# Optimization experiments

Hardware: AMD Instinct MI355X
Metric: run time of the kernel (lower is better)

The kernel has to match this reference:

```python
import jax, jax.numpy as jnp
import numpy as np

B, S, F = 64, 4096, 128      # batch, seq_len, fcnn_unit
RANK, FUSED = 16, 10


def setup_inputs() -> dict:
    key = jax.random.key(0)
    ks = jax.random.split(key, 10)
    xavier = lambda k, shape: jax.random.normal(k, shape, jnp.float32) * np.sqrt(2.0 / (shape[-2] + shape[-1]))
    return {
        "imu_h": jax.random.normal(ks[0], (B, S, F), jnp.float32),
        "vid_h": jax.random.normal(ks[1], (B, S, F), jnp.float32),
        "anthro": jax.random.uniform(ks[2], (B, 1, 2), jnp.float32, 0.5, 1.5),
        "imu_factor": xavier(ks[3], (RANK, 1, F + 1, FUSED)),
        "vid_factor": xavier(ks[4], (RANK, 1, F + 1, FUSED)),
        "fusion_weights": xavier(ks[5], (1, RANK)),
        "fusion_bias": jnp.zeros((1, FUSED), jnp.float32),
        "W1": xavier(ks[6], (FUSED, F)),
        "b1": jnp.zeros((F,), jnp.float32),
        "W2": xavier(ks[7], (F, 2)),
        "b2": jnp.zeros((2,), jnp.float32),
    }


def reference(imu_h, vid_h, anthro, imu_factor, vid_factor,
              fusion_weights, fusion_bias, W1, b1, W2, b2):
    b, s, _ = imu_h.shape
    ones = jnp.ones((b, s, 1), imu_h.dtype)
    _imu_h = jnp.concatenate([ones, imu_h], axis=2)   # [B,S,F+1]
    _vid_h = jnp.concatenate([ones, vid_h], axis=2)
    # torch.matmul([B,S,F+1], [rank,1,F+1,d]) -> [rank,B,S,d]
    fusion_imu = jnp.einsum('bsf,rfd->rbsd', _imu_h, imu_factor[:, 0])
    fusion_vid = jnp.einsum('bsf,rfd->rbsd', _vid_h, vid_factor[:, 0])
    fusion_zy = fusion_imu * fusion_vid               # [rank,B,S,d]
    # weighted combine over rank + bias -> [B,S,d]
    seq = jnp.einsum('r,rbsd->bsd', fusion_weights[0], fusion_zy) + fusion_bias[0]
    seq = jax.nn.relu(seq @ W1 + b1)                  # [B,S,F]
    seq = seq @ W2 + b2                               # [B,S,2]
    wh = (anthro[:, 0, 0] * anthro[:, 0, 1])[:, None, None]  # weight*height
    return seq / wh
```

## Files before the change

### kernel.cpp

```cpp
#include <hip/hip_runtime.h>
#include <hip/hip_bf16.h>
#include <stdint.h>


#define NTOK   262144
#define FDIM   128
#define RANKN  16
#define FUSED  10
#define WTE    (FUSED*RANKN*FDIM)
#define NEXTRA 1984

typedef unsigned short u16;
typedef __bf16 bf16x8 __attribute__((ext_vector_type(8)));
typedef float  f32x4  __attribute__((ext_vector_type(4)));

static __device__ __forceinline__ u16 f2bf(float f) {
    union { float f; uint32_t u; } c; c.f = f;
    uint32_t u = c.u + 0x7FFFu + ((c.u >> 16) & 1u);
    return (u16)(u >> 16);
}

__global__ void prep_kernel(const float* __restrict__ imf, const float* __restrict__ vif,
                            const float* __restrict__ fw,  const float* __restrict__ fb,
                            const float* __restrict__ W1,  const float* __restrict__ b1,
                            const float* __restrict__ W2,
                            u16* __restrict__ wImu, u16* __restrict__ wVid,
                            float* __restrict__ extra) {
    int idx = blockIdx.x * blockDim.x + threadIdx.x;
    float* a0  = extra;
    float* b0  = extra + 160;
    float* W1L = extra + 320;
    float* b1L = extra + 1600;
    float* w20 = extra + 1728;
    float* w21 = extra + 1856;

    if (idx < FUSED * RANKN * FDIM) {
        int k = idx & 127;
        int r = (idx >> 7) & 15;
        int d = idx >> 11;
        int src = r * ((FDIM + 1) * FUSED) + (k + 1) * FUSED + d;
        int kk   = k >> 5;
        int quad = (k >> 3) & 3;
        int j    = k & 7;
        int lane = quad * 16 + r;
        int dst  = ((d * 4 + kk) * 64 + lane) * 8 + j;
        wImu[dst] = f2bf(fw[r] * imf[src]);
        wVid[dst] = f2bf(vif[src]);
    }
    if (idx < RANKN * FUSED) {
        int r = idx & 15, d = idx >> 4;
        int src = r * ((FDIM + 1) * FUSED) + d;
        a0[idx] = fw[r] * imf[src];
        b0[idx] = vif[src];
    }
    if (idx < 1280) {
        int i = idx & 3;
        int t = idx >> 2;
        int d = t % 10;
        int gq = t / 10;
        int g = gq >> 2, q = gq & 3;
        int j = q * 32 + g * 4 + i;
        W1L[idx] = W1[d * FDIM + j];
    }
    if (idx < FDIM) {
        int i = idx & 3;
        int gq = idx >> 2;
        int g = gq >> 2, q = gq & 3;
        int j = q * 32 + g * 4 + i;
        float acc = b1[j];
        #pragma unroll
        for (int d = 0; d < FUSED; ++d) acc += fb[d] * W1[d * FDIM + j];
        b1L[idx] = acc;
        w20[idx] = W2[2 * j];
        w21[idx] = W2[2 * j + 1];
    }
}

__launch_bounds__(512, 2)
__global__ void fusion_main(const float* __restrict__ imu, const float* __restrict__ vid,
                            const float* __restrict__ anthro,
                            const u16* __restrict__ wImuG, const u16* __restrict__ wVidG,
                            const float* __restrict__ extraG,
                            const float* __restrict__ b2g,
                            float* __restrict__ out) {
    extern __shared__ char smem[];
    u16* sFI = (u16*)smem;
    u16* sFV = sFI + WTE;
    float* sX   = (float*)(sFV + WTE);
    float* sA0  = sX;
    float* sB0  = sX + 160;
    float* sW1L = sX + 320;
    float* sB1L = sX + 1600;
    float* sW20 = sX + 1728;
    float* sW21 = sX + 1856;

    {
        const uint4* srcI = (const uint4*)wImuG;
        const uint4* srcV = (const uint4*)wVidG;
        const uint4* srcX = (const uint4*)extraG;
        uint4* dstI = (uint4*)sFI;
        uint4* dstV = (uint4*)sFV;
        uint4* dstX = (uint4*)sX;
        for (int i = threadIdx.x; i < WTE / 8; i += blockDim.x) {
            dstI[i] = srcI[i];
            dstV[i] = srcV[i];
        }
        for (int i = threadIdx.x; i < NEXTRA / 4; i += blockDim.x)
            dstX[i] = srcX[i];
    }

    const int lane = threadIdx.x & 63;
    const int quad = lane >> 4;
    const int r16  = lane & 15;
    const int wid  = threadIdx.x >> 6;
    const int t0   = (blockIdx.x * 8 + wid) * 16;

    const int bidx = t0 >> 12;
    const float invwh = 1.0f / (anthro[2 * bidx] * anthro[2 * bidx + 1]);
    const float b20 = b2g[0], b21 = b2g[1];

    bf16x8 aI[4], aV[4];
    {
        const float* baseI = imu + (size_t)(t0 + r16) * FDIM + quad * 8;
        const float* baseV = vid + (size_t)(t0 + r16) * FDIM + quad * 8;
        #pragma unroll
        for (int kk = 0; kk < 4; ++kk) {
            f32x4 v0 = *(const f32x4*)(baseI + kk * 32);
            f32x4 v1 = *(const f32x4*)(baseI + kk * 32 + 4);
            f32x4 w0 = *(const f32x4*)(baseV + kk * 32);
            f32x4 w1 = *(const f32x4*)(baseV + kk * 32 + 4);
            bf16x8 a, b;
            #pragma unroll
            for (int j = 0; j < 4; ++j) {
                a[j] = (__bf16)v0[j]; a[j + 4] = (__bf16)v1[j];
                b[j] = (__bf16)w0[j]; b[j + 4] = (__bf16)w1[j];
            }
            aI[kk] = a;
            aV[kk] = b;
        }
    }
    __syncthreads();

    const bf16x8* fragI = (const bf16x8*)(const void*)sFI;
    const bf16x8* fragV = (const bf16x8*)(const void*)sFV;

    float seqv[FUSED];
    #pragma unroll
    for (int d = 0; d < FUSED; ++d) {
        f32x4 accU = {0.f, 0.f, 0.f, 0.f};
        f32x4 accV = {0.f, 0.f, 0.f, 0.f};
        #pragma unroll
        for (int kk = 0; kk < 4; ++kk) {
            accU = __builtin_amdgcn_mfma_f32_16x16x32_bf16(fragI[(d * 4 + kk) * 64 + lane], aI[kk], accU, 0, 0, 0);
            accV = __builtin_amdgcn_mfma_f32_16x16x32_bf16(fragV[(d * 4 + kk) * 64 + lane], aV[kk], accV, 0, 0, 0);
        }
        f32x4 a0c = *(const f32x4*)(sA0 + d * 16 + quad * 4);
        f32x4 b0c = *(const f32x4*)(sB0 + d * 16 + quad * 4);
        float s = 0.f;
        #pragma unroll
        for (int reg = 0; reg < 4; ++reg)
            s += (accU[reg] + a0c[reg]) * (accV[reg] + b0c[reg]);
        s += __shfl_xor(s, 16, 64);
        s += __shfl_xor(s, 32, 64);
        seqv[d] = s;
    }

    float o0 = 0.f, o1 = 0.f;
    #pragma unroll
    for (int g = 0; g < 8; ++g) {
        const int gq = g * 4 + quad;
        f32x4 h = *(const f32x4*)(sB1L + gq * 4);
        #pragma unroll
        for (int d = 0; d < FUSED; ++d) {
            f32x4 wv = *(const f32x4*)(sW1L + (gq * 10 + d) * 4);
            #pragma unroll
            for (int i = 0; i < 4; ++i) h[i] += seqv[d] * wv[i];
        }
        f32x4 w20v = *(const f32x4*)(sW20 + gq * 4);
        f32x4 w21v = *(const f32x4*)(sW21 + gq * 4);
        #pragma unroll
        for (int i = 0; i < 4; ++i) {
            float hr = fmaxf(h[i], 0.f);
            o0 += hr * w20v[i];
            o1 += hr * w21v[i];
        }
    }
    o0 += __shfl_xor(o0, 16, 64);
    o0 += __shfl_xor(o0, 32, 64);
    o1 += __shfl_xor(o1, 16, 64);
    o1 += __shfl_xor(o1, 32, 64);

    if (lane < 16) {
        const int t = t0 + r16;
        float2 o = make_float2((o0 + b20) * invwh, (o1 + b21) * invwh);
        *(float2*)(out + 2 * t) = o;
    }
}

extern "C" void kernel_launch(void* const* d_in, const int* in_sizes, int n_in,
                              void* d_out, int out_size, void* d_ws, size_t ws_size,
                              hipStream_t stream) {
    const float* imu    = (const float*)d_in[0];
    const float* vid    = (const float*)d_in[1];
    const float* anthro = (const float*)d_in[2];
    const float* imf    = (const float*)d_in[3];
    const float* vif    = (const float*)d_in[4];
    const float* fw     = (const float*)d_in[5];
    const float* fb     = (const float*)d_in[6];
    const float* W1     = (const float*)d_in[7];
    const float* b1     = (const float*)d_in[8];
    const float* W2     = (const float*)d_in[9];
    const float* b2     = (const float*)d_in[10];
    float* out = (float*)d_out;

    u16* wImu = (u16*)d_ws;
    u16* wVid = wImu + WTE;
    float* extra = (float*)(wVid + WTE);

    prep_kernel<<<80, 256, 0, stream>>>(imf, vif, fw, fb, W1, b1, W2,
                                        wImu, wVid, extra);

    const size_t smem = (size_t)(2 * WTE) * sizeof(u16)
                      + (size_t)NEXTRA * sizeof(float);
    fusion_main<<<2048, 512, smem, stream>>>(imu, vid, anthro, wImu, wVid,
                                             extra, b2, out);
}
```

Before: 318.8 us.

## Switch to 32x32x16 MFMA with 32 tokens per wave

```diff
diff --git a/kernel.cpp b/kernel.cpp
--- a/kernel.cpp
+++ b/kernel.cpp
@@ -13,6 +13,7 @@
 typedef unsigned short u16;
 typedef __bf16 bf16x8 __attribute__((ext_vector_type(8)));
 typedef float  f32x4  __attribute__((ext_vector_type(4)));
+typedef float  f32x16 __attribute__((ext_vector_type(16)));
 
 static __device__ __forceinline__ u16 f2bf(float f) {
     union { float f; uint32_t u; } c; c.f = f;
@@ -35,38 +36,43 @@
     float* w21 = extra + 1856;
 
     if (idx < FUSED * RANKN * FDIM) {
-        int k = idx & 127;
-        int r = (idx >> 7) & 15;
-        int d = idx >> 11;
-        int src = r * ((FDIM + 1) * FUSED) + (k + 1) * FUSED + d;
-        int kk   = k >> 5;
-        int quad = (k >> 3) & 3;
-        int j    = k & 7;
-        int lane = quad * 16 + r;
-        int dst  = ((d * 4 + kk) * 64 + lane) * 8 + j;
-        wImu[dst] = f2bf(fw[r] * imf[src]);
-        wVid[dst] = f2bf(vif[src]);
-    }
-    if (idx < RANKN * FUSED) {
-        int r = idx & 15, d = idx >> 4;
-        int src = r * ((FDIM + 1) * FUSED) + d;
+        int j    = idx & 7;
+        int lane = (idx >> 3) & 63;
+        int ks   = (idx >> 9) & 7;
+        int nt   = idx >> 12;
+        int k    = ks * 16 + (lane >> 5) * 8 + j;
+        int col  = nt * 32 + (lane & 31);
+        int d    = nt * 2 + ((col >> 4) & 1);
+        int r    = col & 15;
+        int src  = r * ((FDIM + 1) * FUSED) + (k + 1) * FUSED + d;
+        wImu[idx] = f2bf(fw[r] * imf[src]);
+        wVid[idx] = f2bf(vif[src]);
+    }
+    if (idx < 160) {
+        int slot = idx & 7;
+        int hi   = (idx >> 3) & 1;
+        int dl   = (idx >> 4) & 1;
+        int nt   = idx >> 5;
+        int d    = nt * 2 + dl;
+        int r    = (slot & 3) + 8 * (slot >> 2) + 4 * hi;
+        int src  = r * ((FDIM + 1) * FUSED) + d;
         a0[idx] = fw[r] * imf[src];
         b0[idx] = vif[src];
     }
     if (idx < 1280) {
-        int i = idx & 3;
-        int t = idx >> 2;
-        int d = t % 10;
+        int i  = idx & 3;
+        int t  = idx >> 2;
+        int d  = t % 10;
         int gq = t / 10;
-        int g = gq >> 2, q = gq & 3;
-        int j = q * 32 + g * 4 + i;
+        int hi = gq >> 4, jg = gq & 15;
+        int j  = hi * 64 + jg * 4 + i;
         W1L[idx] = W1[d * FDIM + j];
     }
     if (idx < FDIM) {
-        int i = idx & 3;
+        int i  = idx & 3;
         int gq = idx >> 2;
-        int g = gq >> 2, q = gq & 3;
-        int j = q * 32 + g * 4 + i;
+        int hi = gq >> 4, jg = gq & 15;
+        int j  = hi * 64 + jg * 4 + i;
         float acc = b1[j];
         #pragma unroll
         for (int d = 0; d < FUSED; ++d) acc += fb[d] * W1[d * FDIM + j];
@@ -76,7 +82,7 @@
     }
 }
 
-__launch_bounds__(512, 2)
+__launch_bounds__(512, 1)
 __global__ void fusion_main(const float* __restrict__ imu, const float* __restrict__ vid,
                             const float* __restrict__ anthro,
                             const u16* __restrict__ wImuG, const u16* __restrict__ wVidG,
@@ -110,33 +116,33 @@
     }
 
     const int lane = threadIdx.x & 63;
-    const int quad = lane >> 4;
-    const int r16  = lane & 15;
+    const int hi   = lane >> 5;
+    const int col  = lane & 31;
     const int wid  = threadIdx.x >> 6;
-    const int t0   = (blockIdx.x * 8 + wid) * 16;
+    const int t0   = (blockIdx.x * 8 + wid) * 32;
 
     const int bidx = t0 >> 12;
     const float invwh = 1.0f / (anthro[2 * bidx] * anthro[2 * bidx + 1]);
     const float b20 = b2g[0], b21 = b2g[1];
 
-    bf16x8 aI[4], aV[4];
+    bf16x8 tI[8], tV[8];
     {
-        const float* baseI = imu + (size_t)(t0 + r16) * FDIM + quad * 8;
-        const float* baseV = vid + (size_t)(t0 + r16) * FDIM + quad * 8;
-        #pragma unroll
-        for (int kk = 0; kk < 4; ++kk) {
-            f32x4 v0 = *(const f32x4*)(baseI + kk * 32);
-            f32x4 v1 = *(const f32x4*)(baseI + kk * 32 + 4);
-            f32x4 w0 = *(const f32x4*)(baseV + kk * 32);
-            f32x4 w1 = *(const f32x4*)(baseV + kk * 32 + 4);
+        const float* baseI = imu + (size_t)(t0 + col) * FDIM + hi * 8;
+        const float* baseV = vid + (size_t)(t0 + col) * FDIM + hi * 8;
+        #pragma unroll
+        for (int ks = 0; ks < 8; ++ks) {
+            f32x4 v0 = *(const f32x4*)(baseI + ks * 16);
+            f32x4 v1 = *(const f32x4*)(baseI + ks * 16 + 4);
+            f32x4 w0 = *(const f32x4*)(baseV + ks * 16);
+            f32x4 w1 = *(const f32x4*)(baseV + ks * 16 + 4);
             bf16x8 a, b;
             #pragma unroll
             for (int j = 0; j < 4; ++j) {
                 a[j] = (__bf16)v0[j]; a[j + 4] = (__bf16)v1[j];
                 b[j] = (__bf16)w0[j]; b[j + 4] = (__bf16)w1[j];
             }
-            aI[kk] = a;
-            aV[kk] = b;
+            tI[ks] = a;
+            tV[ks] = b;
         }
     }
     __syncthreads();
@@ -146,29 +152,40 @@
 
     float seqv[FUSED];
     #pragma unroll
-    for (int d = 0; d < FUSED; ++d) {
-        f32x4 accU = {0.f, 0.f, 0.f, 0.f};
-        f32x4 accV = {0.f, 0.f, 0.f, 0.f};
-        #pragma unroll
-        for (int kk = 0; kk < 4; ++kk) {
-            accU = __builtin_amdgcn_mfma_f32_16x16x32_bf16(fragI[(d * 4 + kk) * 64 + lane], aI[kk], accU, 0, 0, 0);
-            accV = __builtin_amdgcn_mfma_f32_16x16x32_bf16(fragV[(d * 4 + kk) * 64 + lane], aV[kk], accV, 0, 0, 0);
-        }
-        f32x4 a0c = *(const f32x4*)(sA0 + d * 16 + quad * 4);
-        f32x4 b0c = *(const f32x4*)(sB0 + d * 16 + quad * 4);
-        float s = 0.f;
-        #pragma unroll
-        for (int reg = 0; reg < 4; ++reg)
-            s += (accU[reg] + a0c[reg]) * (accV[reg] + b0c[reg]);
-        s += __shfl_xor(s, 16, 64);
-        s += __shfl_xor(s, 32, 64);
-        seqv[d] = s;
+    for (int nt = 0; nt < 5; ++nt) {
+        f32x16 accU = {};
+        f32x16 accV = {};
+        #pragma unroll
+        for (int ks = 0; ks < 8; ++ks) {
+            accU = __builtin_amdgcn_mfma_f32_32x32x16_bf16(fragI[(nt * 8 + ks) * 64 + lane], tI[ks], accU, 0, 0, 0);
+            accV = __builtin_amdgcn_mfma_f32_32x32x16_bf16(fragV[(nt * 8 + ks) * 64 + lane], tV[ks], accV, 0, 0, 0);
+        }
+        f32x4 a00 = *(const f32x4*)(sA0 + nt * 32 + hi * 8);
+        f32x4 a01 = *(const f32x4*)(sA0 + nt * 32 + hi * 8 + 4);
+        f32x4 a10 = *(const f32x4*)(sA0 + nt * 32 + 16 + hi * 8);
+        f32x4 a11 = *(const f32x4*)(sA0 + nt * 32 + 16 + hi * 8 + 4);
+        f32x4 b00 = *(const f32x4*)(sB0 + nt * 32 + hi * 8);
+        f32x4 b01 = *(const f32x4*)(sB0 + nt * 32 + hi * 8 + 4);
+        f32x4 b10 = *(const f32x4*)(sB0 + nt * 32 + 16 + hi * 8);
+        f32x4 b11 = *(const f32x4*)(sB0 + nt * 32 + 16 + hi * 8 + 4);
+        float s0 = 0.f, s1 = 0.f;
+        #pragma unroll
+        for (int q = 0; q < 4; ++q) {
+            s0 += (accU[q]      + a00[q]) * (accV[q]      + b00[q]);
+            s0 += (accU[q + 4]  + a01[q]) * (accV[q + 4]  + b01[q]);
+            s1 += (accU[q + 8]  + a10[q]) * (accV[q + 8]  + b10[q]);
+            s1 += (accU[q + 12] + a11[q]) * (accV[q + 12] + b11[q]);
+        }
+        s0 += __shfl_xor(s0, 32, 64);
+        s1 += __shfl_xor(s1, 32, 64);
+        seqv[nt * 2]     = s0;
+        seqv[nt * 2 + 1] = s1;
     }
 
     float o0 = 0.f, o1 = 0.f;
     #pragma unroll
-    for (int g = 0; g < 8; ++g) {
-        const int gq = g * 4 + quad;
+    for (int jg = 0; jg < 16; ++jg) {
+        const int gq = hi * 16 + jg;
         f32x4 h = *(const f32x4*)(sB1L + gq * 4);
         #pragma unroll
         for (int d = 0; d < FUSED; ++d) {
@@ -185,13 +202,11 @@
             o1 += hr * w21v[i];
         }
     }
-    o0 += __shfl_xor(o0, 16, 64);
     o0 += __shfl_xor(o0, 32, 64);
-    o1 += __shfl_xor(o1, 16, 64);
     o1 += __shfl_xor(o1, 32, 64);
 
-    if (lane < 16) {
-        const int t = t0 + r16;
+    if (hi == 0) {
+        const int t = t0 + col;
         float2 o = make_float2((o0 + b20) * invwh, (o1 + b21) * invwh);
         *(float2*)(out + 2 * t) = o;
     }
@@ -222,6 +237,6 @@
 
     const size_t smem = (size_t)(2 * WTE) * sizeof(u16)
                       + (size_t)NEXTRA * sizeof(float);
-    fusion_main<<<2048, 512, smem, stream>>>(imu, vid, anthro, wImu, wVid,
+    fusion_main<<<1024, 512, smem, stream>>>(imu, vid, anthro, wImu, wVid,
                                              extra, b2, out);
 }
```

Measured after the change: 357.0 us. 1.12x slower.
